# Kernel tuning notes

Hardware: AMD Instinct MI355X
Metric: run time of the kernel (lower is better)

Reference implementation:

```python
import jax, jax.numpy as jnp
import numpy as np

N = 100000          # nodes
E = 3200000         # directed edges
NUM_GRAPHS = 2000   # pooled segments
D = 64              # hidden dim
L = 3               # num_unit GCNConv layers


def setup_inputs() -> dict:
    key = jax.random.key(0)
    ks = jax.random.split(key, 12)
    x = jax.random.normal(ks[0], (N, 4), dtype=jnp.float32)
    edge_index = jax.random.randint(ks[1], (2, E), 0, N, dtype=jnp.int64)
    batch = jnp.sort(jax.random.randint(ks[2], (N,), 0, NUM_GRAPHS, dtype=jnp.int64))
    def lin(k, out_f, in_f):
        kw, kb = jax.random.split(k)
        lim = 1.0 / np.sqrt(in_f)
        W = jax.random.uniform(kw, (out_f, in_f), jnp.float32, -lim, lim)
        b = jax.random.uniform(kb, (out_f,), jnp.float32, -lim, lim)
        return W, b
    emb_w, emb_b = lin(ks[3], D, 4)
    cw, cb = [], []
    for i in range(L):
        W, b = lin(ks[4 + i], D, D)
        cw.append(W); cb.append(b)
    conv_w = jnp.stack(cw)   # [L, D, D]
    conv_b = jnp.stack(cb)   # [L, D]
    lin1_w, lin1_b = lin(ks[8], D, D)
    lin2_w, lin2_b = lin(ks[9], 3, D)
    return {"x": x, "edge_index": edge_index, "batch": batch,
            "emb_w": emb_w, "emb_b": emb_b, "conv_w": conv_w, "conv_b": conv_b,
            "lin1_w": lin1_w, "lin1_b": lin1_b, "lin2_w": lin2_w, "lin2_b": lin2_b}


def reference(x, edge_index, batch, emb_w, emb_b, conv_w, conv_b,
              lin1_w, lin1_b, lin2_w, lin2_b):
    # ---- GCN normalization (edge_weight = 1, self-loops added, shared across layers) ----
    loop = jnp.arange(N, dtype=edge_index.dtype)
    src = jnp.concatenate([edge_index[0], loop])   # [E+N]
    dst = jnp.concatenate([edge_index[1], loop])
    deg = jax.ops.segment_sum(jnp.ones_like(src, dtype=x.dtype), dst, num_segments=N)
    dinv = jnp.where(deg > 0, jax.lax.rsqrt(deg), 0.0)
    norm = dinv[src] * dinv[dst]                   # [E+N]

    # node embedding (dropout in eval mode = identity)
    h = x @ emb_w.T + emb_b                        # [N, D]

    # stacked GCNConv + ReLU: h' = scatter_add(norm * (h W^T)[src] -> dst) + b
    for l in range(L):
        t = h @ conv_w[l].T                        # [N, D]
        msg = t[src] * norm[:, None]               # gather + scale, [E+N, D]
        h = jax.ops.segment_sum(msg, dst, num_segments=N) + conv_b[l]
        h = jax.nn.relu(h)

    # global mean pool over graphs
    gsum = jax.ops.segment_sum(h, batch, num_segments=NUM_GRAPHS)        # [G, D]
    cnt = jax.ops.segment_sum(jnp.ones((N,), x.dtype), batch, num_segments=NUM_GRAPHS)
    gmean = gsum / jnp.maximum(cnt, 1.0)[:, None]

    # MLP head
    p = jax.nn.relu(gmean @ lin1_w.T + lin1_b)
    pred = p @ lin2_w.T + lin2_b                   # [G, 3]
    return pred
```

## Files before the change

### kernel.cpp

```cpp
#include <hip/hip_runtime.h>

__device__ __forceinline__ unsigned short f2bf(float f) {
    union { float f; unsigned int u; } c; c.f = f;
    unsigned int r = c.u + 0x7fffu + ((c.u >> 16) & 1u);
    return (unsigned short)(r >> 16);
}
__device__ __forceinline__ float bflo(unsigned int v) {
    union { unsigned int u; float f; } c; c.u = v << 16; return c.f;
}
__device__ __forceinline__ float bfhi(unsigned int v) {
    union { unsigned int u; float f; } c; c.u = v & 0xffff0000u; return c.f;
}


#define BIN_CAP 10240
#define NBINS_MAX 1024

__global__ __launch_bounds__(1024) void k_binA(const int* __restrict__ src,
                                               const int* __restrict__ dst,
                                               int* __restrict__ bincntPad,
                                               int* __restrict__ bincntExact,
                                               int* __restrict__ binbuf,
                                               int E, int nbins) {
    __shared__ int hist[NBINS_MAX];
    __shared__ int lbase[NBINS_MAX];
    int tid = threadIdx.x;
    int chunk = (E + gridDim.x - 1) / gridDim.x;
    int e0 = blockIdx.x * chunk;
    int e1 = min(e0 + chunk, E);

    for (int i = tid; i < nbins; i += 1024) hist[i] = 0;
    __syncthreads();
    for (int e = e0 + tid; e < e1; e += 1024) atomicAdd(&hist[dst[e] >> 7], 1);
    __syncthreads();
    for (int i = tid; i < nbins; i += 1024) {
        int c = hist[i];
        if (c) {
            atomicAdd(&bincntExact[i], c);
            lbase[i] = atomicAdd(&bincntPad[i], (c + 15) & ~15);
        }
        hist[i] = 0;
    }
    __syncthreads();
    for (int e = e0 + tid; e < e1; e += 1024) {
        int d = dst[e], s = src[e];
        int b = d >> 7;
        int pos = lbase[b] + atomicAdd(&hist[b], 1);
        binbuf[(size_t)b * BIN_CAP + pos] = ((d & 127) << 20) | s;
    }
    __syncthreads();
    for (int i = tid; i < nbins; i += 1024) {
        int c = hist[i];
        if (c & 15) {
            int* p = binbuf + (size_t)i * BIN_CAP + lbase[i] + c;
            int pad = 16 - (c & 15);
            for (int j = 0; j < pad; j++) p[j] = 0x7FFFFFFF;
        }
    }
}

__global__ void k_scanB(const int* __restrict__ cntE, int* __restrict__ binstart,
                        int nbins) {
    __shared__ int s[1024];
    int tid = threadIdx.x;
    int v = (tid < nbins) ? cntE[tid] : 0;
    s[tid] = v;
    __syncthreads();
    for (int off = 1; off < 1024; off <<= 1) {
        int t = (tid >= off) ? s[tid - off] : 0;
        __syncthreads();
        s[tid] += t;
        __syncthreads();
    }
    if (tid < nbins) binstart[tid] = s[tid] - v;
}

__global__ __launch_bounds__(512) void k_binC(const int* __restrict__ bincntPad,
                                              const int* __restrict__ binstart,
                                              const int* __restrict__ binbuf,
                                              int* __restrict__ deg,
                                              float* __restrict__ dinv,
                                              int* __restrict__ rowptr,
                                              int* __restrict__ col, int n) {
    __shared__ int hist[128];
    __shared__ int scn[128];
    __shared__ int cur[128];
    int b = blockIdx.x, tid = threadIdx.x;
    int cnt = bincntPad[b];
    const int* rec = binbuf + (size_t)b * BIN_CAP;
    if (tid < 128) hist[tid] = 0;
    __syncthreads();
    for (int i = tid * 4; i + 3 < cnt; i += 2048) {
        int4 r4 = *(const int4*)&rec[i];
        if ((r4.x & 0xFFFFF) < n) atomicAdd(&hist[(r4.x >> 20) & 127], 1);
        if ((r4.y & 0xFFFFF) < n) atomicAdd(&hist[(r4.y >> 20) & 127], 1);
        if ((r4.z & 0xFFFFF) < n) atomicAdd(&hist[(r4.z >> 20) & 127], 1);
        if ((r4.w & 0xFFFFF) < n) atomicAdd(&hist[(r4.w >> 20) & 127], 1);
    }
    __syncthreads();
    int v = (tid < 128) ? hist[tid] : 0;
    if (tid < 128) scn[tid] = v;
    __syncthreads();
    for (int off = 1; off < 128; off <<= 1) {
        int t = (tid < 128 && tid >= off) ? scn[tid - off] : 0;
        __syncthreads();
        if (tid < 128) scn[tid] += t;
        __syncthreads();
    }
    int rowbase = binstart[b];
    if (tid < 128) {
        int excl = scn[tid] - v;
        cur[tid] = rowbase + excl;
        int node = b * 128 + tid;
        if (node < n) {
            deg[node] = v;
            dinv[node] = rsqrtf((float)(v + 1));
            rowptr[node] = rowbase + excl;
        }
    }
    __syncthreads();
    for (int i = tid * 4; i + 3 < cnt; i += 2048) {
        int4 r4 = *(const int4*)&rec[i];
        int s0 = r4.x & 0xFFFFF, s1 = r4.y & 0xFFFFF;
        int s2 = r4.z & 0xFFFFF, s3 = r4.w & 0xFFFFF;
        if (s0 < n) col[atomicAdd(&cur[(r4.x >> 20) & 127], 1)] = s0;
        if (s1 < n) col[atomicAdd(&cur[(r4.y >> 20) & 127], 1)] = s1;
        if (s2 < n) col[atomicAdd(&cur[(r4.z >> 20) & 127], 1)] = s2;
        if (s3 < n) col[atomicAdd(&cur[(r4.w >> 20) & 127], 1)] = s3;
    }
}


__global__ __launch_bounds__(256) void k_gemm0(const float* __restrict__ x,
                                               const float* __restrict__ embw,
                                               const float* __restrict__ embb,
                                               const float* __restrict__ W,
                                               const float* __restrict__ dinv,
                                               unsigned short* __restrict__ uout, int n) {
    __shared__ float hN[64 * 68];
    __shared__ float wT[64 * 68];
    __shared__ float sX[64 * 4];
    __shared__ float sW[64 * 4];
    __shared__ float sB[64];
    int tid = threadIdx.x;
    int nbase = blockIdx.x * 64;
    for (int i = tid; i < 4096; i += 256) {
        int j = i >> 6, k = i & 63;
        wT[k * 68 + j] = W[i];
    }
    if (tid < 256) sW[tid] = embw[tid];
    if (tid < 64) sB[tid] = embb[tid];
    {
        int node = nbase + (tid >> 2);
        sX[tid] = (node < n) ? x[(size_t)node * 4 + (tid & 3)] : 0.f;
    }
    __syncthreads();
    for (int i = tid; i < 4096; i += 256) {
        int nn = i >> 6, k = i & 63;
        float s = sB[k];
        s = fmaf(sX[nn * 4 + 0], sW[k * 4 + 0], s);
        s = fmaf(sX[nn * 4 + 1], sW[k * 4 + 1], s);
        s = fmaf(sX[nn * 4 + 2], sW[k * 4 + 2], s);
        s = fmaf(sX[nn * 4 + 3], sW[k * 4 + 3], s);
        hN[nn * 68 + k] = s;
    }
    __syncthreads();

    int tx = tid & 15;
    int ty = tid >> 4;
    float acc[4][4] = {};
#pragma unroll
    for (int k0 = 0; k0 < 64; k0 += 4) {
        float a[4][4], w[4][4];
#pragma unroll
        for (int i = 0; i < 4; i++)
            *(float4*)a[i] = *(const float4*)&hN[(ty * 4 + i) * 68 + k0];
#pragma unroll
        for (int dk = 0; dk < 4; dk++)
            *(float4*)w[dk] = *(const float4*)&wT[(k0 + dk) * 68 + tx * 4];
#pragma unroll
        for (int i = 0; i < 4; i++)
#pragma unroll
            for (int j = 0; j < 4; j++)
#pragma unroll
                for (int dk = 0; dk < 4; dk++)
                    acc[i][j] = fmaf(a[i][dk], w[dk][j], acc[i][j]);
    }
#pragma unroll
    for (int i = 0; i < 4; i++) {
        int node = nbase + ty * 4 + i;
        if (node < n) {
            float sc = dinv[node];
            ushort4 o;
            o.x = f2bf(acc[i][0] * sc);
            o.y = f2bf(acc[i][1] * sc);
            o.z = f2bf(acc[i][2] * sc);
            o.w = f2bf(acc[i][3] * sc);
            *(ushort4*)&uout[(size_t)node * 64 + tx * 4] = o;
        }
    }
}

__global__ __launch_bounds__(256) void k_gemm(const unsigned short* __restrict__ hin,
                                              const float* __restrict__ W,
                                              const float* __restrict__ dinv,
                                              unsigned short* __restrict__ uout, int n) {
    __shared__ float hN[64 * 68];
    __shared__ float wT[64 * 68];
    int tid = threadIdx.x;
    int nbase = blockIdx.x * 64;
    for (int i = tid; i < 4096; i += 256) {
        int j = i >> 6, k = i & 63;
        wT[k * 68 + j] = W[i];
    }
    for (int i = tid; i < 2048; i += 256) {
        int nn = i >> 5, k2 = i & 31;
        int node = nbase + nn;
        unsigned int v = (node < n) ? ((const unsigned int*)hin)[(size_t)node * 32 + k2] : 0u;
        hN[nn * 68 + k2 * 2 + 0] = bflo(v);
        hN[nn * 68 + k2 * 2 + 1] = bfhi(v);
    }
    __syncthreads();

    int tx = tid & 15;
    int ty = tid >> 4;
    float acc[4][4] = {};
#pragma unroll
    for (int k0 = 0; k0 < 64; k0 += 4) {
        float a[4][4], w[4][4];
#pragma unroll
        for (int i = 0; i < 4; i++)
            *(float4*)a[i] = *(const float4*)&hN[(ty * 4 + i) * 68 + k0];
#pragma unroll
        for (int dk = 0; dk < 4; dk++)
            *(float4*)w[dk] = *(const float4*)&wT[(k0 + dk) * 68 + tx * 4];
#pragma unroll
        for (int i = 0; i < 4; i++)
#pragma unroll
            for (int j = 0; j < 4; j++)
#pragma unroll
                for (int dk = 0; dk < 4; dk++)
                    acc[i][j] = fmaf(a[i][dk], w[dk][j], acc[i][j]);
    }
#pragma unroll
    for (int i = 0; i < 4; i++) {
        int node = nbase + ty * 4 + i;
        if (node < n) {
            float sc = dinv[node];
            ushort4 o;
            o.x = f2bf(acc[i][0] * sc);
            o.y = f2bf(acc[i][1] * sc);
            o.z = f2bf(acc[i][2] * sc);
            o.w = f2bf(acc[i][3] * sc);
            *(ushort4*)&uout[(size_t)node * 64 + tx * 4] = o;
        }
    }
}

__global__ void k_agg(const unsigned short* __restrict__ u, const int* __restrict__ rowptr,
                      const int* __restrict__ deg, const int* __restrict__ col,
                      const float* __restrict__ dinv, const float* __restrict__ bias,
                      unsigned short* __restrict__ hout, int n) {
    int wid = (blockIdx.x * blockDim.x + threadIdx.x) >> 6;
    int lane = threadIdx.x & 63;
    if (wid >= n) return;
    int g = lane >> 4, t = lane & 15;
    const unsigned int* u32 = (const unsigned int*)u;
    const int toff = t * 2;

    float a0 = 0.f, a1 = 0.f, a2 = 0.f, a3 = 0.f;
    if (g == 0) {
        uint2 v = *(const uint2*)&u32[(size_t)wid * 32 + toff];
        a0 = bflo(v.x); a1 = bfhi(v.x); a2 = bflo(v.y); a3 = bfhi(v.y);
    }
    int p0 = rowptr[wid];
    int e = p0 + deg[wid];
    int p = p0 + g;
    for (; p + 12 < e; p += 16) {
        int s0 = col[p], s1 = col[p + 4], s2 = col[p + 8], s3 = col[p + 12];
        uint2 v0 = *(const uint2*)&u32[(size_t)s0 * 32 + toff];
        uint2 v1 = *(const uint2*)&u32[(size_t)s1 * 32 + toff];
        uint2 v2 = *(const uint2*)&u32[(size_t)s2 * 32 + toff];
        uint2 v3 = *(const uint2*)&u32[(size_t)s3 * 32 + toff];
        a0 += bflo(v0.x); a1 += bfhi(v0.x); a2 += bflo(v0.y); a3 += bfhi(v0.y);
        a0 += bflo(v1.x); a1 += bfhi(v1.x); a2 += bflo(v1.y); a3 += bfhi(v1.y);
        a0 += bflo(v2.x); a1 += bfhi(v2.x); a2 += bflo(v2.y); a3 += bfhi(v2.y);
        a0 += bflo(v3.x); a1 += bfhi(v3.x); a2 += bflo(v3.y); a3 += bfhi(v3.y);
    }
    for (; p < e; p += 4) {
        int s0 = col[p];
        uint2 v0 = *(const uint2*)&u32[(size_t)s0 * 32 + toff];
        a0 += bflo(v0.x); a1 += bfhi(v0.x); a2 += bflo(v0.y); a3 += bfhi(v0.y);
    }
    a0 += __shfl_xor(a0, 16, 64); a1 += __shfl_xor(a1, 16, 64);
    a2 += __shfl_xor(a2, 16, 64); a3 += __shfl_xor(a3, 16, 64);
    a0 += __shfl_xor(a0, 32, 64); a1 += __shfl_xor(a1, 32, 64);
    a2 += __shfl_xor(a2, 32, 64); a3 += __shfl_xor(a3, 32, 64);

    if (g == 0) {
        float sc = dinv[wid];
        float f0 = fmaxf(fmaf(sc, a0, bias[t * 4 + 0]), 0.f);
        float f1 = fmaxf(fmaf(sc, a1, bias[t * 4 + 1]), 0.f);
        float f2 = fmaxf(fmaf(sc, a2, bias[t * 4 + 2]), 0.f);
        float f3 = fmaxf(fmaf(sc, a3, bias[t * 4 + 3]), 0.f);
        ushort4 o;
        o.x = f2bf(f0); o.y = f2bf(f1); o.z = f2bf(f2); o.w = f2bf(f3);
        *(ushort4*)&hout[(size_t)wid * 64 + t * 4] = o;
    }
}

__global__ __launch_bounds__(256) void k_pool(const unsigned short* __restrict__ h,
                                              const int* __restrict__ batch,
                                              const float* __restrict__ l1w,
                                              const float* __restrict__ l1b,
                                              const float* __restrict__ l2w,
                                              const float* __restrict__ l2b,
                                              float* __restrict__ out, int n, int G) {
    __shared__ float wl[64 * 65];
    __shared__ float gsm[4][64];
    int tid = threadIdx.x;
    for (int i = tid; i < 4096; i += 256) {
        int j = i >> 6, k = i & 63;
        wl[j * 65 + k] = l1w[i];
    }
    int wv = tid >> 6;
    int lane = tid & 63;
    int g = blockIdx.x * 4 + wv;
    int grp = lane >> 4, t = lane & 15;
    const unsigned int* h32 = (const unsigned int*)h;

    int start = 0, end = 0;
    if (g < G) {
        int lo = 0, hi = n;
        while (lo < hi) { int mid = (lo + hi) >> 1; if (batch[mid] < g) lo = mid + 1; else hi = mid; }
        start = lo;
        hi = n;
        while (lo < hi) { int mid = (lo + hi) >> 1; if (batch[mid] < g + 1) lo = mid + 1; else hi = mid; }
        end = lo;
    }

    float a0 = 0.f, a1 = 0.f, a2 = 0.f, a3 = 0.f;
    int nb = start;
    for (; nb + 4 <= end; nb += 4) {
        int node = nb + grp;
        uint2 v = *(const uint2*)&h32[(size_t)node * 32 + t * 2];
        a0 += bflo(v.x); a1 += bfhi(v.x); a2 += bflo(v.y); a3 += bfhi(v.y);
    }
    if (grp < end - nb) {
        int node = nb + grp;
        uint2 v = *(const uint2*)&h32[(size_t)node * 32 + t * 2];
        a0 += bflo(v.x); a1 += bfhi(v.x); a2 += bflo(v.y); a3 += bfhi(v.y);
    }
    a0 += __shfl_xor(a0, 16, 64); a1 += __shfl_xor(a1, 16, 64);
    a2 += __shfl_xor(a2, 16, 64); a3 += __shfl_xor(a3, 16, 64);
    a0 += __shfl_xor(a0, 32, 64); a1 += __shfl_xor(a1, 32, 64);
    a2 += __shfl_xor(a2, 32, 64); a3 += __shfl_xor(a3, 32, 64);

    float cnt = (float)((end - start) > 0 ? (end - start) : 1);
    if (grp == 0) {
        gsm[wv][t * 4 + 0] = a0 / cnt;
        gsm[wv][t * 4 + 1] = a1 / cnt;
        gsm[wv][t * 4 + 2] = a2 / cnt;
        gsm[wv][t * 4 + 3] = a3 / cnt;
    }
    __syncthreads();
    if (g < G) {
        float pj = l1b[lane];
#pragma unroll
        for (int k = 0; k < 64; k++) pj = fmaf(gsm[wv][k], wl[lane * 65 + k], pj);
        pj = fmaxf(pj, 0.f);
        for (int o = 0; o < 3; o++) {
            float v = pj * l2w[o * 64 + lane];
            for (int off = 32; off; off >>= 1) v += __shfl_xor(v, off, 64);
            if (lane == 0) out[g * 3 + o] = v + l2b[o];
        }
    }
}


extern "C" void kernel_launch(void* const* d_in, const int* in_sizes, int n_in,
                              void* d_out, int out_size, void* d_ws, size_t ws_size,
                              hipStream_t stream) {
    const float* x      = (const float*)d_in[0];
    const int*   edge   = (const int*)d_in[1];
    const int*   batch  = (const int*)d_in[2];
    const float* emb_w  = (const float*)d_in[3];
    const float* emb_b  = (const float*)d_in[4];
    const float* conv_w = (const float*)d_in[5];
    const float* conv_b = (const float*)d_in[6];
    const float* l1w    = (const float*)d_in[7];
    const float* l1b    = (const float*)d_in[8];
    const float* l2w    = (const float*)d_in[9];
    const float* l2b    = (const float*)d_in[10];
    float* out = (float*)d_out;

    const int N = in_sizes[2];
    const int E = in_sizes[1] / 2;
    const int G = out_size / 3;
    const int NB = (N + 127) >> 7;

    char* ws = (char*)d_ws;
    size_t off = 0;
    auto alloc = [&](size_t bytes) -> void* {
        void* p = ws + off;
        off = (off + bytes + 255) & ~(size_t)255;
        return p;
    };
    int*   deg      = (int*)alloc((size_t)N * 4);
    float* dinv     = (float*)alloc((size_t)N * 4);
    int*   rowptr   = (int*)alloc((size_t)N * 4);
    int*   bincntP  = (int*)alloc((size_t)NB * 4);
    int*   bincntE  = (int*)alloc((size_t)NB * 4);
    int*   binstart = (int*)alloc((size_t)NB * 4);
    int*   colw     = (int*)alloc((size_t)E * 4);
    int*   binbuf   = (int*)alloc((size_t)NB * BIN_CAP * 4);
    unsigned short* ubuf = (unsigned short*)binbuf;
    unsigned short* hbuf = (unsigned short*)((char*)binbuf + (size_t)N * 64 * 2);

    const int* esrc = edge;
    const int* edst = edge + E;

    hipMemsetAsync(bincntP, 0, (size_t)((char*)bincntE - (char*)bincntP) + (size_t)NB * 4, stream);
    k_binA<<<256, 1024, 0, stream>>>(esrc, edst, bincntP, bincntE, binbuf, E, NB);
    k_scanB<<<1, 1024, 0, stream>>>(bincntE, binstart, NB);
    k_binC<<<NB, 512, 0, stream>>>(bincntP, binstart, binbuf, deg, dinv, rowptr, colw, N);

    k_gemm0<<<(N + 63) / 64, 256, 0, stream>>>(x, emb_w, emb_b, conv_w, dinv, ubuf, N);
    k_agg<<<(N + 3) / 4, 256, 0, stream>>>(ubuf, rowptr, deg, colw, dinv, conv_b, hbuf, N);
    for (int l = 1; l < 3; l++) {
        k_gemm<<<(N + 63) / 64, 256, 0, stream>>>(hbuf, conv_w + (size_t)l * 64 * 64, dinv, ubuf, N);
        k_agg<<<(N + 3) / 4, 256, 0, stream>>>(ubuf, rowptr, deg, colw, dinv, conv_b + (size_t)l * 64, hbuf, N);
    }

    k_pool<<<(G + 3) / 4, 256, 0, stream>>>(hbuf, batch, l1w, l1b, l2w, l2b, out, N, G);
}
```

Before: 449.3 us.

## Sort CSR columns into source slices and aggregate slice-by-slice across nodes

The CSR build now splits each destination's neighbour list into 8 sub-ranges keyed by source-node region and writes a per-slice row pointer array. The aggregation kernel has each 16-lane group handle 5 nodes and walk all of them through one source slice before moving to the next, so that concurrent gathers hit a narrower region of the feature table and reuse cache lines better. Column indices are loaded cooperatively and broadcast with shuffles instead of per-lane scalar loads. The trade-off is a larger scan in the binning kernel, a smaller bin capacity, and more loop and branch overhead per node.

```diff
diff --git a/kernel.cpp b/kernel.cpp
--- a/kernel.cpp
+++ b/kernel.cpp
@@ -13,7 +13,7 @@
 }
 
 
-#define BIN_CAP 10240
+#define BIN_CAP 8192
 #define NBINS_MAX 1024
 
 __global__ __launch_bounds__(1024) void k_binA(const int* __restrict__ src,
@@ -75,58 +75,59 @@
     if (tid < nbins) binstart[tid] = s[tid] - v;
 }
 
-__global__ __launch_bounds__(512) void k_binC(const int* __restrict__ bincntPad,
-                                              const int* __restrict__ binstart,
-                                              const int* __restrict__ binbuf,
-                                              int* __restrict__ deg,
-                                              float* __restrict__ dinv,
-                                              int* __restrict__ rowptr,
-                                              int* __restrict__ col, int n) {
-    __shared__ int hist[128];
-    __shared__ int scn[128];
-    __shared__ int cur[128];
+__global__ __launch_bounds__(1024) void k_binC(const int* __restrict__ bincntPad,
+                                               const int* __restrict__ binstart,
+                                               const int* __restrict__ binbuf,
+                                               float* __restrict__ dinv,
+                                               int* __restrict__ rowptrS,
+                                               int* __restrict__ col, int n) {
+    __shared__ int hist[1024];
+    __shared__ int scn[1024];
+    __shared__ int cur[1024];
     int b = blockIdx.x, tid = threadIdx.x;
     int cnt = bincntPad[b];
     const int* rec = binbuf + (size_t)b * BIN_CAP;
-    if (tid < 128) hist[tid] = 0;
-    __syncthreads();
-    for (int i = tid * 4; i + 3 < cnt; i += 2048) {
+    hist[tid] = 0;
+    __syncthreads();
+    for (int i = tid * 4; i + 3 < cnt; i += 4096) {
         int4 r4 = *(const int4*)&rec[i];
-        if ((r4.x & 0xFFFFF) < n) atomicAdd(&hist[(r4.x >> 20) & 127], 1);
-        if ((r4.y & 0xFFFFF) < n) atomicAdd(&hist[(r4.y >> 20) & 127], 1);
-        if ((r4.z & 0xFFFFF) < n) atomicAdd(&hist[(r4.z >> 20) & 127], 1);
-        if ((r4.w & 0xFFFFF) < n) atomicAdd(&hist[(r4.w >> 20) & 127], 1);
-    }
-    __syncthreads();
-    int v = (tid < 128) ? hist[tid] : 0;
-    if (tid < 128) scn[tid] = v;
-    __syncthreads();
-    for (int off = 1; off < 128; off <<= 1) {
-        int t = (tid < 128 && tid >= off) ? scn[tid - off] : 0;
+        int s;
+        s = r4.x & 0xFFFFF; if (s < n) atomicAdd(&hist[((r4.x >> 20) & 127) * 8 + (s >> 14)], 1);
+        s = r4.y & 0xFFFFF; if (s < n) atomicAdd(&hist[((r4.y >> 20) & 127) * 8 + (s >> 14)], 1);
+        s = r4.z & 0xFFFFF; if (s < n) atomicAdd(&hist[((r4.z >> 20) & 127) * 8 + (s >> 14)], 1);
+        s = r4.w & 0xFFFFF; if (s < n) atomicAdd(&hist[((r4.w >> 20) & 127) * 8 + (s >> 14)], 1);
+    }
+    __syncthreads();
+    int v = hist[tid];
+    scn[tid] = v;
+    __syncthreads();
+    for (int off = 1; off < 1024; off <<= 1) {
+        int t = (tid >= off) ? scn[tid - off] : 0;
         __syncthreads();
-        if (tid < 128) scn[tid] += t;
+        scn[tid] += t;
         __syncthreads();
     }
     int rowbase = binstart[b];
+    int excl = rowbase + scn[tid] - v;
+    cur[tid] = excl;
+    rowptrS[(size_t)b * 1024 + tid] = excl;
     if (tid < 128) {
-        int excl = scn[tid] - v;
-        cur[tid] = rowbase + excl;
         int node = b * 128 + tid;
         if (node < n) {
-            deg[node] = v;
-            dinv[node] = rsqrtf((float)(v + 1));
-            rowptr[node] = rowbase + excl;
-        }
-    }
-    __syncthreads();
-    for (int i = tid * 4; i + 3 < cnt; i += 2048) {
+            int deg = 0;
+#pragma unroll
+            for (int k2 = 0; k2 < 8; k2++) deg += hist[tid * 8 + k2];
+            dinv[node] = rsqrtf((float)(deg + 1));
+        }
+    }
+    __syncthreads();
+    for (int i = tid * 4; i + 3 < cnt; i += 4096) {
         int4 r4 = *(const int4*)&rec[i];
-        int s0 = r4.x & 0xFFFFF, s1 = r4.y & 0xFFFFF;
-        int s2 = r4.z & 0xFFFFF, s3 = r4.w & 0xFFFFF;
-        if (s0 < n) col[atomicAdd(&cur[(r4.x >> 20) & 127], 1)] = s0;
-        if (s1 < n) col[atomicAdd(&cur[(r4.y >> 20) & 127], 1)] = s1;
-        if (s2 < n) col[atomicAdd(&cur[(r4.z >> 20) & 127], 1)] = s2;
-        if (s3 < n) col[atomicAdd(&cur[(r4.w >> 20) & 127], 1)] = s3;
+        int s;
+        s = r4.x & 0xFFFFF; if (s < n) col[atomicAdd(&cur[((r4.x >> 20) & 127) * 8 + (s >> 14)], 1)] = s;
+        s = r4.y & 0xFFFFF; if (s < n) col[atomicAdd(&cur[((r4.y >> 20) & 127) * 8 + (s >> 14)], 1)] = s;
+        s = r4.z & 0xFFFFF; if (s < n) col[atomicAdd(&cur[((r4.z >> 20) & 127) * 8 + (s >> 14)], 1)] = s;
+        s = r4.w & 0xFFFFF; if (s < n) col[atomicAdd(&cur[((r4.w >> 20) & 127) * 8 + (s >> 14)], 1)] = s;
     }
 }
 
@@ -257,55 +258,83 @@
     }
 }
 
-__global__ void k_agg(const unsigned short* __restrict__ u, const int* __restrict__ rowptr,
-                      const int* __restrict__ deg, const int* __restrict__ col,
-                      const float* __restrict__ dinv, const float* __restrict__ bias,
-                      unsigned short* __restrict__ hout, int n) {
-    int wid = (blockIdx.x * blockDim.x + threadIdx.x) >> 6;
-    int lane = threadIdx.x & 63;
-    if (wid >= n) return;
+#define NPB 80
+__global__ __launch_bounds__(256) void k_agg(const unsigned short* __restrict__ u,
+                                             const int* __restrict__ rowptrS,
+                                             const int* __restrict__ col,
+                                             const float* __restrict__ dinv,
+                                             const float* __restrict__ bias,
+                                             unsigned short* __restrict__ hout, int n) {
+    int tid = threadIdx.x;
+    int wave = tid >> 6, lane = tid & 63;
     int g = lane >> 4, t = lane & 15;
+    int gb = g << 4;
+    int wbase = blockIdx.x * NPB + wave * (NPB / 4);
     const unsigned int* u32 = (const unsigned int*)u;
     const int toff = t * 2;
 
-    float a0 = 0.f, a1 = 0.f, a2 = 0.f, a3 = 0.f;
-    if (g == 0) {
-        uint2 v = *(const uint2*)&u32[(size_t)wid * 32 + toff];
-        a0 = bflo(v.x); a1 = bfhi(v.x); a2 = bflo(v.y); a3 = bfhi(v.y);
-    }
-    int p0 = rowptr[wid];
-    int e = p0 + deg[wid];
-    int p = p0 + g;
-    for (; p + 12 < e; p += 16) {
-        int s0 = col[p], s1 = col[p + 4], s2 = col[p + 8], s3 = col[p + 12];
-        uint2 v0 = *(const uint2*)&u32[(size_t)s0 * 32 + toff];
-        uint2 v1 = *(const uint2*)&u32[(size_t)s1 * 32 + toff];
-        uint2 v2 = *(const uint2*)&u32[(size_t)s2 * 32 + toff];
-        uint2 v3 = *(const uint2*)&u32[(size_t)s3 * 32 + toff];
-        a0 += bflo(v0.x); a1 += bfhi(v0.x); a2 += bflo(v0.y); a3 += bfhi(v0.y);
-        a0 += bflo(v1.x); a1 += bfhi(v1.x); a2 += bflo(v1.y); a3 += bfhi(v1.y);
-        a0 += bflo(v2.x); a1 += bfhi(v2.x); a2 += bflo(v2.y); a3 += bfhi(v2.y);
-        a0 += bflo(v3.x); a1 += bfhi(v3.x); a2 += bflo(v3.y); a3 += bfhi(v3.y);
-    }
-    for (; p < e; p += 4) {
-        int s0 = col[p];
-        uint2 v0 = *(const uint2*)&u32[(size_t)s0 * 32 + toff];
-        a0 += bflo(v0.x); a1 += bfhi(v0.x); a2 += bflo(v0.y); a3 += bfhi(v0.y);
-    }
-    a0 += __shfl_xor(a0, 16, 64); a1 += __shfl_xor(a1, 16, 64);
-    a2 += __shfl_xor(a2, 16, 64); a3 += __shfl_xor(a3, 16, 64);
-    a0 += __shfl_xor(a0, 32, 64); a1 += __shfl_xor(a1, 32, 64);
-    a2 += __shfl_xor(a2, 32, 64); a3 += __shfl_xor(a3, 32, 64);
-
-    if (g == 0) {
-        float sc = dinv[wid];
-        float f0 = fmaxf(fmaf(sc, a0, bias[t * 4 + 0]), 0.f);
-        float f1 = fmaxf(fmaf(sc, a1, bias[t * 4 + 1]), 0.f);
-        float f2 = fmaxf(fmaf(sc, a2, bias[t * 4 + 2]), 0.f);
-        float f3 = fmaxf(fmaf(sc, a3, bias[t * 4 + 3]), 0.f);
-        ushort4 o;
-        o.x = f2bf(f0); o.y = f2bf(f1); o.z = f2bf(f2); o.w = f2bf(f3);
-        *(ushort4*)&hout[(size_t)wid * 64 + t * 4] = o;
+    float acc[5][4] = {};
+    int segp[5];
+#pragma unroll
+    for (int i = 0; i < 5; i++) {
+        int node = wbase + i * 4 + g;
+        segp[i] = (node < n) ? rowptrS[node * 8] : 0;
+    }
+#pragma unroll 1
+    for (int sl = 0; sl < 8; sl++) {
+#pragma unroll
+        for (int i = 0; i < 5; i++) {
+            int node = wbase + i * 4 + g;
+            if (node >= n) continue;
+            int pend = rowptrS[node * 8 + sl + 1];
+            int p = segp[i];
+            segp[i] = pend;
+            while (p < pend) {
+                int m = min(pend - p, 16);
+                int cv = (t < m) ? col[p + t] : 0;
+                int e = 0;
+                for (; e + 3 < m; e += 4) {
+                    int s0 = __shfl(cv, gb + e + 0, 64);
+                    int s1 = __shfl(cv, gb + e + 1, 64);
+                    int s2 = __shfl(cv, gb + e + 2, 64);
+                    int s3 = __shfl(cv, gb + e + 3, 64);
+                    uint2 v0 = *(const uint2*)&u32[(size_t)s0 * 32 + toff];
+                    uint2 v1 = *(const uint2*)&u32[(size_t)s1 * 32 + toff];
+                    uint2 v2 = *(const uint2*)&u32[(size_t)s2 * 32 + toff];
+                    uint2 v3 = *(const uint2*)&u32[(size_t)s3 * 32 + toff];
+                    acc[i][0] += bflo(v0.x); acc[i][1] += bfhi(v0.x);
+                    acc[i][2] += bflo(v0.y); acc[i][3] += bfhi(v0.y);
+                    acc[i][0] += bflo(v1.x); acc[i][1] += bfhi(v1.x);
+                    acc[i][2] += bflo(v1.y); acc[i][3] += bfhi(v1.y);
+                    acc[i][0] += bflo(v2.x); acc[i][1] += bfhi(v2.x);
+                    acc[i][2] += bflo(v2.y); acc[i][3] += bfhi(v2.y);
+                    acc[i][0] += bflo(v3.x); acc[i][1] += bfhi(v3.x);
+                    acc[i][2] += bflo(v3.y); acc[i][3] += bfhi(v3.y);
+                }
+                for (; e < m; e++) {
+                    int s0 = __shfl(cv, gb + e, 64);
+                    uint2 v0 = *(const uint2*)&u32[(size_t)s0 * 32 + toff];
+                    acc[i][0] += bflo(v0.x); acc[i][1] += bfhi(v0.x);
+                    acc[i][2] += bflo(v0.y); acc[i][3] += bfhi(v0.y);
+                }
+                p += m;
+            }
+        }
+    }
+#pragma unroll
+    for (int i = 0; i < 5; i++) {
+        int node = wbase + i * 4 + g;
+        if (node < n) {
+            uint2 sv = *(const uint2*)&u32[(size_t)node * 32 + toff];
+            float sc = dinv[node];
+            float f0 = fmaxf(fmaf(sc, acc[i][0] + bflo(sv.x), bias[t * 4 + 0]), 0.f);
+            float f1 = fmaxf(fmaf(sc, acc[i][1] + bfhi(sv.x), bias[t * 4 + 1]), 0.f);
+            float f2 = fmaxf(fmaf(sc, acc[i][2] + bflo(sv.y), bias[t * 4 + 2]), 0.f);
+            float f3 = fmaxf(fmaf(sc, acc[i][3] + bfhi(sv.y), bias[t * 4 + 3]), 0.f);
+            ushort4 o;
+            o.x = f2bf(f0); o.y = f2bf(f1); o.z = f2bf(f2); o.w = f2bf(f3);
+            *(ushort4*)&hout[(size_t)node * 64 + t * 4] = o;
+        }
     }
 }
 
@@ -406,13 +435,12 @@
         off = (off + bytes + 255) & ~(size_t)255;
         return p;
     };
-    int*   deg      = (int*)alloc((size_t)N * 4);
     float* dinv     = (float*)alloc((size_t)N * 4);
-    int*   rowptr   = (int*)alloc((size_t)N * 4);
     int*   bincntP  = (int*)alloc((size_t)NB * 4);
     int*   bincntE  = (int*)alloc((size_t)NB * 4);
     int*   binstart = (int*)alloc((size_t)NB * 4);
     int*   colw     = (int*)alloc((size_t)E * 4);
+    int*   rowptrS  = (int*)alloc(((size_t)NB * 1024 + 8) * 4);
     int*   binbuf   = (int*)alloc((size_t)NB * BIN_CAP * 4);
     unsigned short* ubuf = (unsigned short*)binbuf;
     unsigned short* hbuf = (unsigned short*)((char*)binbuf + (size_t)N * 64 * 2);
@@ -423,13 +451,15 @@
     hipMemsetAsync(bincntP, 0, (size_t)((char*)bincntE - (char*)bincntP) + (size_t)NB * 4, stream);
     k_binA<<<256, 1024, 0, stream>>>(esrc, edst, bincntP, bincntE, binbuf, E, NB);
     k_scanB<<<1, 1024, 0, stream>>>(bincntE, binstart, NB);
-    k_binC<<<NB, 512, 0, stream>>>(bincntP, binstart, binbuf, deg, dinv, rowptr, colw, N);
-
+    k_binC<<<NB, 1024, 0, stream>>>(bincntP, binstart, binbuf, dinv, rowptrS, colw, N);
+
+    int aggBlocks = (N + NPB - 1) / NPB;
     k_gemm0<<<(N + 63) / 64, 256, 0, stream>>>(x, emb_w, emb_b, conv_w, dinv, ubuf, N);
-    k_agg<<<(N + 3) / 4, 256, 0, stream>>>(ubuf, rowptr, deg, colw, dinv, conv_b, hbuf, N);
+    k_agg<<<aggBlocks, 256, 0, stream>>>(ubuf, rowptrS, colw, dinv, conv_b, hbuf, N);
     for (int l = 1; l < 3; l++) {
         k_gemm<<<(N + 63) / 64, 256, 0, stream>>>(hbuf, conv_w + (size_t)l * 64 * 64, dinv, ubuf, N);
-        k_agg<<<(N + 3) / 4, 256, 0, stream>>>(ubuf, rowptr, deg, colw, dinv, conv_b + (size_t)l * 64, hbuf, N);
+        k_agg<<<aggBlocks, 256, 0, stream>>>(ubuf, rowptrS, colw, dinv,
+                                             conv_b + (size_t)l * 64, hbuf, N);
     }
 
     k_pool<<<(G + 3) / 4, 256, 0, stream>>>(hbuf, batch, l1w, l1b, l2w, l2b, out, N, G);
```

Result: slower. 520.3 us (+15.8%).
